# Kernel tuning notes

Hardware: AMD Instinct MI355X
Metric: run time of the kernel (lower is better)

## Reference

```python
import jax, jax.numpy as jnp
import numpy as np

B, C, N, M, K = 1, 64, 65536, 65536, 16
H, O = 64, 128  # mlp hidden, out_channels


def setup_inputs() -> dict:
    key = jax.random.key(0)
    ks = jax.random.split(key, 8)
    return {
        "x": jax.random.normal(ks[0], (B, C, N), dtype=jnp.float32),
        "pos": jax.random.normal(ks[1], (B, 3, N), dtype=jnp.float32),
        "support_points": jax.random.normal(ks[2], (B, 3, M), dtype=jnp.float32),
        "W1": jax.random.normal(ks[3], (H, C + 3), dtype=jnp.float32) * 0.05,
        "b1": jax.random.normal(ks[4], (H,), dtype=jnp.float32) * 0.05,
        "W2": jax.random.normal(ks[5], (O, H), dtype=jnp.float32) * 0.05,
        "b2": jax.random.normal(ks[6], (O,), dtype=jnp.float32) * 0.05,
        "indices": jax.random.randint(ks[7], (B, M, K), 0, N, dtype=jnp.int64),
    }


def _gather_points(t, indices):
    # t: [B, C, N], indices: [B, M, K] -> [B, C, M, K]
    b, c, n = t.shape
    m, k = indices.shape[1], indices.shape[2]
    idx = indices.reshape(b, 1, m * k)  # broadcasts over channel dim
    return jnp.take_along_axis(t, idx, axis=2).reshape(b, c, m, k)


def reference(x, pos, support_points, W1, b1, W2, b2, indices):
    # gather neighbor features and positions: [B, C, M, K], [B, 3, M, K]
    feats = _gather_points(x, indices)
    pts = _gather_points(pos, indices) - support_points[:, :, :, None]
    h = jnp.concatenate([feats, pts], axis=1)  # [B, C+3, M, K]
    # shared per-point MLP (1x1 Conv2d == channel contraction)
    h = jnp.einsum("oc,bcmk->bomk", W1, h) + b1[None, :, None, None]
    h = jax.nn.relu(h)
    h = jnp.einsum("oc,bcmk->bomk", W2, h) + b2[None, :, None, None]
    # max-pool over neighborhood K -> [B, O, M]
    return jnp.max(h, axis=3)
```

## Files before the change

kernel.cpp:

```cpp
#include <hip/hip_runtime.h>
#include <hip/hip_bf16.h>

#define NPTS 65536
#define MPTS 65536

typedef __attribute__((ext_vector_type(8))) short bf16x8;
typedef __attribute__((ext_vector_type(4))) float f32x4;

__device__ __forceinline__ float bflo(unsigned int u){ union{unsigned int i; float f;} v; v.i = u<<16; return v.f; }
__device__ __forceinline__ float bfhi(unsigned int u){ union{unsigned int i; float f;} v; v.i = u & 0xffff0000u; return v.f; }
__device__ __forceinline__ unsigned short f2bf(float f){
  union{float f; unsigned int i;} v; v.f=f;
  unsigned int r = v.i + 0x7fffu + ((v.i>>16)&1u);
  return (unsigned short)(r>>16);
}
__device__ __forceinline__ unsigned int pk2f(float a, float b){
  float2 tf; tf.x = a; tf.y = b;
  union { __hip_bfloat162 h; unsigned int u; } c;
  c.h = __float22bfloat162_rn(tf);
  return c.u;
}

#define MFMA32(a,b,c) __builtin_amdgcn_mfma_f32_16x16x32_bf16((a),(b),(c),0,0,0)

__global__ __launch_bounds__(256) void pack_u(
    const float* __restrict__ x,
    const float* __restrict__ pos,
    const float* __restrict__ sup,
    const float* __restrict__ W1,
    const float* __restrict__ b1,
    const float* __restrict__ W2,
    unsigned short* __restrict__ U,
    unsigned short* __restrict__ W2F,
    float* __restrict__ V) {
  const int t = threadIdx.x;
  if (blockIdx.x >= 1028) {
    const int m = (blockIdx.x - 1028) * 256 + t;
    const float s0 = sup[m], s1 = sup[MPTS + m], s2 = sup[2*MPTS + m];
    #pragma unroll
    for (int cg = 0; cg < 16; ++cg) {
      const float* r0 = W1 + (size_t)(cg*4 + 0)*67 + 64;
      const float* r1 = W1 + (size_t)(cg*4 + 1)*67 + 64;
      const float* r2 = W1 + (size_t)(cg*4 + 2)*67 + 64;
      const float* r3 = W1 + (size_t)(cg*4 + 3)*67 + 64;
      float4 o;
      o.x = r0[0]*s0 + r0[1]*s1 + r0[2]*s2;
      o.y = r1[0]*s0 + r1[1]*s1 + r1[2]*s2;
      o.z = r2[0]*s0 + r2[1]*s1 + r2[2]*s2;
      o.w = r3[0]*s0 + r3[1]*s1 + r3[2]*s2;
      *(float4*)(V + (size_t)m*64 + cg*4) = o;
    }
    return;
  }
  if (blockIdx.x >= 1024) {
    const int gg = (blockIdx.x - 1024) * 256 + t;
    if (gg < 1024) {
      const int g = gg >> 6, lane = gg & 63;
      const int q = lane >> 4, lr = lane & 15;
      const int kt = g >> 3, ot = g & 7;
      #pragma unroll
      for (int j = 0; j < 4; ++j)
        *(unsigned int*)&W2F[gg*8 + 2*j] =
            pk2f(W2[(ot*16 + lr)*64 + kt*32 + q*8 + 2*j],
                 W2[(ot*16 + lr)*64 + kt*32 + q*8 + 2*j + 1]);
    }
    return;
  }
  const int lane = t & 63, w = t >> 6, quad = lane >> 4, lr = lane & 15;
  const int n = blockIdx.x * 64 + w * 16 + lr;

  bf16x8 wa[2][4], wt[4];
  #pragma unroll
  for (int kt = 0; kt < 2; ++kt)
    #pragma unroll
    for (int nt = 0; nt < 4; ++nt) {
      const float* r = W1 + (size_t)(nt*16 + lr)*67 + kt*32 + quad*8;
      const float4 a = *(const float4*)r;
      const float4 b = *(const float4*)(r + 4);
      union { unsigned int d[4]; bf16x8 v; } mk;
      mk.d[0] = pk2f(a.x, a.y); mk.d[1] = pk2f(a.z, a.w);
      mk.d[2] = pk2f(b.x, b.y); mk.d[3] = pk2f(b.z, b.w);
      wa[kt][nt] = mk.v;
    }
  #pragma unroll
  for (int nt = 0; nt < 4; ++nt) {
    union { unsigned int d[4]; bf16x8 v; } mk;
    mk.d[0] = 0u; mk.d[1] = 0u; mk.d[2] = 0u; mk.d[3] = 0u;
    if (quad == 0) {
      const float* r = W1 + (size_t)(nt*16 + lr)*67 + 64;
      mk.d[0] = pk2f(r[0], r[1]);
      mk.d[1] = (unsigned int)f2bf(r[2]);
    }
    wt[nt] = mk.v;
  }

  const f32x4 fz = {0.f, 0.f, 0.f, 0.f};
  f32x4 acc[4] = {fz, fz, fz, fz};
  #pragma unroll
  for (int kt = 0; kt < 2; ++kt) {
    const float* xc = x + (size_t)(kt*32 + quad*8) * NPTS + n;
    union { unsigned int d[4]; bf16x8 v; } mk;
    #pragma unroll
    for (int i = 0; i < 4; ++i)
      mk.d[i] = pk2f(xc[(size_t)(2*i) * NPTS], xc[(size_t)(2*i + 1) * NPTS]);
    #pragma unroll
    for (int nt = 0; nt < 4; ++nt)
      acc[nt] = MFMA32(wa[kt][nt], mk.v, acc[nt]);
  }
  {
    union { unsigned int d[4]; bf16x8 v; } mk;
    mk.d[0] = pk2f(pos[n], pos[NPTS + n]);
    mk.d[1] = (unsigned int)f2bf(pos[2*NPTS + n]);
    mk.d[2] = 0u; mk.d[3] = 0u;
    #pragma unroll
    for (int nt = 0; nt < 4; ++nt)
      acc[nt] = MFMA32(wt[nt], mk.v, acc[nt]);
  }
  #pragma unroll
  for (int nt = 0; nt < 4; ++nt) {
    const float4 bb = *(const float4*)(b1 + nt*16 + quad*4);
    uint2 d;
    d.x = pk2f(acc[nt][0] + bb.x, acc[nt][1] + bb.y);
    d.y = pk2f(acc[nt][2] + bb.z, acc[nt][3] + bb.w);
    *(uint2*)(U + (size_t)n * 64 + nt*16 + quad*4) = d;
  }
}

__global__ __launch_bounds__(256, 3) void pointnet_reg2(
    const unsigned short* __restrict__ U,
    const float* __restrict__ V,
    const unsigned short* __restrict__ W2F,
    const float* __restrict__ b2,
    const int* __restrict__ indices,
    float* __restrict__ out) {
  const int t = threadIdx.x;
  const int lane = t & 63, w = t >> 6, quad = lane >> 4, lr = lane & 15;
  const int wbase = blockIdx.x * 32 + w * 8;

  int idx[8];
  #pragma unroll
  for (int pt = 0; pt < 8; ++pt) idx[pt] = indices[(wbase + pt)*16 + lr];

  uint4 ur[8][2];
  #pragma unroll
  for (int pt = 0; pt < 8; ++pt)
    #pragma unroll
    for (int kt = 0; kt < 2; ++kt)
      ur[pt][kt] = *(const uint4*)(U + (size_t)idx[pt]*64 + kt*32 + quad*8);

  bf16x8 ah[8][2];
  #pragma unroll
  for (int pt = 0; pt < 8; ++pt) {
    const float* vr = V + (size_t)(wbase + pt)*64 + quad*8;
    float vv[16];
    *(float4*)&vv[0]  = *(const float4*)(vr);
    *(float4*)&vv[4]  = *(const float4*)(vr + 4);
    *(float4*)&vv[8]  = *(const float4*)(vr + 32);
    *(float4*)&vv[12] = *(const float4*)(vr + 36);
    #pragma unroll
    for (int kt = 0; kt < 2; ++kt) {
      const unsigned int uu[4] = {ur[pt][kt].x, ur[pt][kt].y, ur[pt][kt].z, ur[pt][kt].w};
      union { unsigned int d[4]; bf16x8 v; } mk;
      #pragma unroll
      for (int i = 0; i < 4; ++i) {
        const float lo = bflo(uu[i]) - vv[kt*8 + 2*i];
        const float hi = bfhi(uu[i]) - vv[kt*8 + 2*i + 1];
        mk.d[i] = pk2f(fmaxf(lo, 0.f), fmaxf(hi, 0.f));
      }
      ah[pt][kt] = mk.v;
    }
  }

  const f32x4 fz = {0.f, 0.f, 0.f, 0.f};
  #pragma unroll
  for (int ot = 0; ot < 8; ++ot) {
    const bf16x8 wb0 = ((const bf16x8*)W2F)[(0*8 + ot)*64 + lane];
    const bf16x8 wb1 = ((const bf16x8*)W2F)[(1*8 + ot)*64 + lane];
    float vm[8];
    #pragma unroll
    for (int pt = 0; pt < 8; ++pt) {
      f32x4 a2 = MFMA32(ah[pt][0], wb0, fz);
      a2 = MFMA32(ah[pt][1], wb1, a2);
      float v = fmaxf(fmaxf(a2[0], a2[1]), fmaxf(a2[2], a2[3]));
      v = fmaxf(v, __int_as_float(__builtin_amdgcn_ds_swizzle(__float_as_int(v), 0x401F)));
      v = fmaxf(v, __shfl_xor(v, 32));
      vm[pt] = v;
    }
    const int o = ot*16 + lr;
    const float bb = b2[o];
    const float va = (quad & 1) ? ((quad & 2) ? vm[3] : vm[1])
                                : ((quad & 2) ? vm[2] : vm[0]);
    const float vb = (quad & 1) ? ((quad & 2) ? vm[7] : vm[5])
                                : ((quad & 2) ? vm[6] : vm[4]);
    out[(size_t)o * MPTS + wbase + quad] = va + bb;
    out[(size_t)o * MPTS + wbase + 4 + quad] = vb + bb;
  }
}

__global__ __launch_bounds__(256, 3) void pointnet_reg(
    const unsigned short* __restrict__ U,
    const float* __restrict__ sup,
    const float* __restrict__ W1,
    const unsigned short* __restrict__ W2F,
    const float* __restrict__ b2,
    const int* __restrict__ indices,
    float* __restrict__ out) {
  const int t = threadIdx.x;
  const int lane = t & 63, w = t >> 6, quad = lane >> 4, lr = lane & 15;
  const int wbase = blockIdx.x * 32 + w * 8;

  int idx[8];
  #pragma unroll
  for (int pt = 0; pt < 8; ++pt) idx[pt] = indices[(wbase + pt)*16 + lr];

  uint4 ur[8][2];
  #pragma unroll
  for (int pt = 0; pt < 8; ++pt)
    #pragma unroll
    for (int kt = 0; kt < 2; ++kt)
      ur[pt][kt] = *(const uint4*)(U + (size_t)idx[pt]*64 + kt*32 + quad*8);

  bf16x8 ah[8][2];
  #pragma unroll
  for (int kt = 0; kt < 2; ++kt) {
    float w1p[8][3];
    #pragma unroll
    for (int j = 0; j < 8; ++j) {
      const float* r = W1 + (size_t)(kt*32 + quad*8 + j)*67 + 64;
      w1p[j][0] = r[0]; w1p[j][1] = r[1]; w1p[j][2] = r[2];
    }
    #pragma unroll
    for (int pt = 0; pt < 8; ++pt) {
      const float s0 = sup[wbase + pt];
      const float s1 = sup[MPTS + wbase + pt];
      const float s2 = sup[2*MPTS + wbase + pt];
      const unsigned int uu[4] = {ur[pt][kt].x, ur[pt][kt].y, ur[pt][kt].z, ur[pt][kt].w};
      union { unsigned int d[4]; bf16x8 v; } mk;
      #pragma unroll
      for (int i = 0; i < 4; ++i) {
        const float vl = w1p[2*i][0]*s0 + w1p[2*i][1]*s1 + w1p[2*i][2]*s2;
        const float vh = w1p[2*i+1][0]*s0 + w1p[2*i+1][1]*s1 + w1p[2*i+1][2]*s2;
        const float hl = fmaxf(bflo(uu[i]) - vl, 0.f);
        const float hh = fmaxf(bfhi(uu[i]) - vh, 0.f);
        mk.d[i] = pk2f(hl, hh);
      }
      ah[pt][kt] = mk.v;
    }
  }

  const f32x4 fz = {0.f, 0.f, 0.f, 0.f};
  #pragma unroll
  for (int ot = 0; ot < 8; ++ot) {
    const bf16x8 wb0 = ((const bf16x8*)W2F)[(0*8 + ot)*64 + lane];
    const bf16x8 wb1 = ((const bf16x8*)W2F)[(1*8 + ot)*64 + lane];
    float vm[8];
    #pragma unroll
    for (int pt = 0; pt < 8; ++pt) {
      f32x4 a2 = MFMA32(ah[pt][0], wb0, fz);
      a2 = MFMA32(ah[pt][1], wb1, a2);
      float v = fmaxf(fmaxf(a2[0], a2[1]), fmaxf(a2[2], a2[3]));
      v = fmaxf(v, __shfl_xor(v, 16));
      v = fmaxf(v, __shfl_xor(v, 32));
      vm[pt] = v;
    }
    const int o = ot*16 + lr;
    const float bb = b2[o];
    const float va = (quad & 1) ? ((quad & 2) ? vm[3] : vm[1])
                                : ((quad & 2) ? vm[2] : vm[0]);
    const float vb = (quad & 1) ? ((quad & 2) ? vm[7] : vm[5])
                                : ((quad & 2) ? vm[6] : vm[4]);
    out[(size_t)o * MPTS + wbase + quad] = va + bb;
    out[(size_t)o * MPTS + wbase + 4 + quad] = vb + bb;
  }
}

__global__ __launch_bounds__(256) void pointnet_fallback(
    const float* __restrict__ x, const float* __restrict__ pos,
    const float* __restrict__ sup,
    const float* __restrict__ W1, const float* __restrict__ b1,
    const float* __restrict__ W2, const float* __restrict__ b2,
    const int* __restrict__ indices, float* __restrict__ out) {
  __shared__ float sfeat[16][68];
  __shared__ float shid[16][64];
  __shared__ float smax[4][128];
  __shared__ int sidx[16];
  const int t = threadIdx.x;
  const int m = blockIdx.x;
  if (t < 16) sidx[t] = indices[m*16 + t];
  const float sup0 = sup[m], sup1 = sup[MPTS + m], sup2 = sup[2*MPTS + m];
  __syncthreads();
  for (int u = t; u < 16*17; u += 256) {
    const int k = u / 17, c4 = (u - k*17) * 4;
    const int idx = sidx[k];
    float4 wv;
    if (c4 < 64) {
      wv.x = x[(size_t)(c4+0)*NPTS + idx]; wv.y = x[(size_t)(c4+1)*NPTS + idx];
      wv.z = x[(size_t)(c4+2)*NPTS + idx]; wv.w = x[(size_t)(c4+3)*NPTS + idx];
    } else {
      wv.x = pos[idx] - sup0; wv.y = pos[NPTS + idx] - sup1;
      wv.z = pos[2*NPTS + idx] - sup2; wv.w = 0.f;
    }
    *(float4*)&sfeat[k][c4] = wv;
  }
  const int h = t & 63, kg = t >> 6;
  float w1r[68];
  #pragma unroll
  for (int c = 0; c < 67; ++c) w1r[c] = W1[h*67 + c];
  w1r[67] = 0.f;
  const float bias1 = b1[h];
  __syncthreads();
  #pragma unroll
  for (int j = 0; j < 4; ++j) {
    const int k = kg*4 + j;
    float a = bias1;
    const float4* rr = (const float4*)sfeat[k];
    #pragma unroll
    for (int qq = 0; qq < 17; ++qq) {
      const float4 v = rr[qq];
      a += w1r[qq*4+0]*v.x + w1r[qq*4+1]*v.y + w1r[qq*4+2]*v.z + w1r[qq*4+3]*v.w;
    }
    shid[k][h] = fmaxf(a, 0.f);
  }
  const int ow = t & 63;
  float w2a[64], w2b[64];
  #pragma unroll
  for (int hh = 0; hh < 64; ++hh) { w2a[hh] = W2[ow*64 + hh]; w2b[hh] = W2[(ow+64)*64 + hh]; }
  __syncthreads();
  float mxa = -3.0e38f, mxb = -3.0e38f;
  #pragma unroll
  for (int j = 0; j < 4; ++j) {
    const int k = kg*4 + j;
    const float4* hr = (const float4*)shid[k];
    float pa = 0.f, pb = 0.f;
    #pragma unroll
    for (int qq = 0; qq < 16; ++qq) {
      const float4 v = hr[qq];
      pa += w2a[qq*4+0]*v.x + w2a[qq*4+1]*v.y + w2a[qq*4+2]*v.z + w2a[qq*4+3]*v.w;
      pb += w2b[qq*4+0]*v.x + w2b[qq*4+1]*v.y + w2b[qq*4+2]*v.z + w2b[qq*4+3]*v.w;
    }
    mxa = fmaxf(mxa, pa); mxb = fmaxf(mxb, pb);
  }
  smax[kg][ow] = mxa; smax[kg][64 + ow] = mxb;
  __syncthreads();
  if (t < 128) {
    out[(size_t)t * MPTS + m] =
        fmaxf(fmaxf(smax[0][t], smax[1][t]), fmaxf(smax[2][t], smax[3][t])) + b2[t];
  }
}

extern "C" void kernel_launch(void* const* d_in, const int* in_sizes, int n_in,
                              void* d_out, int out_size, void* d_ws, size_t ws_size,
                              hipStream_t stream) {
  const float* x   = (const float*)d_in[0];
  const float* pos = (const float*)d_in[1];
  const float* sup = (const float*)d_in[2];
  const float* W1  = (const float*)d_in[3];
  const float* b1  = (const float*)d_in[4];
  const float* W2  = (const float*)d_in[5];
  const float* b2  = (const float*)d_in[6];
  const int* indices = (const int*)d_in[7];
  float* out = (float*)d_out;

  const size_t U_BYTES   = (size_t)NPTS * 64 * 2;
  const size_t W2F_BYTES = 16 * 64 * 8 * 2;
  const size_t V_BYTES   = (size_t)MPTS * 64 * 4;
  if (ws_size >= U_BYTES + W2F_BYTES + V_BYTES) {
    unsigned short* U   = (unsigned short*)d_ws;
    unsigned short* W2F = (unsigned short*)((char*)d_ws + U_BYTES);
    float* V            = (float*)((char*)d_ws + U_BYTES + W2F_BYTES);
    pack_u<<<1028 + 256, 256, 0, stream>>>(x, pos, sup, W1, b1, W2, U, W2F, V);
    pointnet_reg2<<<MPTS/32, 256, 0, stream>>>(U, V, W2F, b2, indices, out);
  } else if (ws_size >= U_BYTES + W2F_BYTES) {
    unsigned short* U   = (unsigned short*)d_ws;
    unsigned short* W2F = (unsigned short*)((char*)d_ws + U_BYTES);
    pack_u<<<1028, 256, 0, stream>>>(x, pos, sup, W1, b1, W2, U, W2F, nullptr);
    pointnet_reg<<<MPTS/32, 256, 0, stream>>>(U, sup, W1, W2F, b2, indices, out);
  } else {
    pointnet_fallback<<<MPTS, 256, 0, stream>>>(x, pos, sup, W1, b1, W2, b2, indices, out);
  }
}
```

Measured before the change: 139.9 us.

## Split pack kernel, stage x/V tiles through LDS, vectorize output stores

```diff
diff --git a/kernel.cpp b/kernel.cpp
--- a/kernel.cpp
+++ b/kernel.cpp
@@ -26,34 +26,98 @@
 __global__ __launch_bounds__(256) void pack_u(
     const float* __restrict__ x,
     const float* __restrict__ pos,
+    const float* __restrict__ W1,
+    const float* __restrict__ b1,
+    unsigned short* __restrict__ U)
+{
+  __shared__ float sx[67][65];
+  const int t = threadIdx.x;
+  const int n0 = blockIdx.x * 64;
+
+  #pragma unroll
+  for (int i = 0; i < 4; ++i) {
+    const int lin = i*256 + t, r = lin >> 4, c4 = (lin & 15) * 4;
+    const float4 v = *(const float4*)&x[(size_t)r * NPTS + n0 + c4];
+    *(float4*)&sx[r][c4] = v;
+  }
+  if (t < 48) {
+    const int lin = 1024 + t, r = lin >> 4, c4 = (lin & 15) * 4;
+    const float4 v = *(const float4*)&pos[(size_t)(r - 64) * NPTS + n0 + c4];
+    *(float4*)&sx[r][c4] = v;
+  }
+
+  const int lane = t & 63, w = t >> 6, quad = lane >> 4, lr = lane & 15;
+  const int col = w * 16 + lr;
+  const int n = n0 + col;
+
+  bf16x8 wa[2][4], wt[4];
+  #pragma unroll
+  for (int kt = 0; kt < 2; ++kt)
+    #pragma unroll
+    for (int nt = 0; nt < 4; ++nt) {
+      const float* r = W1 + (size_t)(nt*16 + lr)*67 + kt*32 + quad*8;
+      const float4 a = *(const float4*)r;
+      const float4 b = *(const float4*)(r + 4);
+      union { unsigned int d[4]; bf16x8 v; } mk;
+      mk.d[0] = pk2f(a.x, a.y); mk.d[1] = pk2f(a.z, a.w);
+      mk.d[2] = pk2f(b.x, b.y); mk.d[3] = pk2f(b.z, b.w);
+      wa[kt][nt] = mk.v;
+    }
+  #pragma unroll
+  for (int nt = 0; nt < 4; ++nt) {
+    union { unsigned int d[4]; bf16x8 v; } mk;
+    mk.d[0] = 0u; mk.d[1] = 0u; mk.d[2] = 0u; mk.d[3] = 0u;
+    if (quad == 0) {
+      const float* r = W1 + (size_t)(nt*16 + lr)*67 + 64;
+      mk.d[0] = pk2f(r[0], r[1]);
+      mk.d[1] = (unsigned int)f2bf(r[2]);
+    }
+    wt[nt] = mk.v;
+  }
+
+  __syncthreads();
+
+  const f32x4 fz = {0.f, 0.f, 0.f, 0.f};
+  f32x4 acc[4] = {fz, fz, fz, fz};
+  #pragma unroll
+  for (int kt = 0; kt < 2; ++kt) {
+    const int c0 = kt*32 + quad*8;
+    union { unsigned int d[4]; bf16x8 v; } mk;
+    #pragma unroll
+    for (int i = 0; i < 4; ++i)
+      mk.d[i] = pk2f(sx[c0 + 2*i][col], sx[c0 + 2*i + 1][col]);
+    #pragma unroll
+    for (int nt = 0; nt < 4; ++nt)
+      acc[nt] = MFMA32(wa[kt][nt], mk.v, acc[nt]);
+  }
+  {
+    union { unsigned int d[4]; bf16x8 v; } mk;
+    mk.d[0] = pk2f(sx[64][col], sx[65][col]);
+    mk.d[1] = (unsigned int)f2bf(sx[66][col]);
+    mk.d[2] = 0u; mk.d[3] = 0u;
+    #pragma unroll
+    for (int nt = 0; nt < 4; ++nt)
+      acc[nt] = MFMA32(wt[nt], mk.v, acc[nt]);
+  }
+  #pragma unroll
+  for (int nt = 0; nt < 4; ++nt) {
+    const float4 bb = *(const float4*)(b1 + nt*16 + quad*4);
+    uint2 d;
+    d.x = pk2f(acc[nt][0] + bb.x, acc[nt][1] + bb.y);
+    d.y = pk2f(acc[nt][2] + bb.z, acc[nt][3] + bb.w);
+    *(uint2*)(U + (size_t)n * 64 + nt*16 + quad*4) = d;
+  }
+}
+
+__global__ __launch_bounds__(256) void pack_aux(
     const float* __restrict__ sup,
     const float* __restrict__ W1,
-    const float* __restrict__ b1,
     const float* __restrict__ W2,
-    unsigned short* __restrict__ U,
-    unsigned short* __restrict__ W2F,
-    float* __restrict__ V) {
+    float* __restrict__ V,
+    unsigned short* __restrict__ W2F) {
   const int t = threadIdx.x;
-  if (blockIdx.x >= 1028) {
-    const int m = (blockIdx.x - 1028) * 256 + t;
-    const float s0 = sup[m], s1 = sup[MPTS + m], s2 = sup[2*MPTS + m];
-    #pragma unroll
-    for (int cg = 0; cg < 16; ++cg) {
-      const float* r0 = W1 + (size_t)(cg*4 + 0)*67 + 64;
-      const float* r1 = W1 + (size_t)(cg*4 + 1)*67 + 64;
-      const float* r2 = W1 + (size_t)(cg*4 + 2)*67 + 64;
-      const float* r3 = W1 + (size_t)(cg*4 + 3)*67 + 64;
-      float4 o;
-      o.x = r0[0]*s0 + r0[1]*s1 + r0[2]*s2;
-      o.y = r1[0]*s0 + r1[1]*s1 + r1[2]*s2;
-      o.z = r2[0]*s0 + r2[1]*s1 + r2[2]*s2;
-      o.w = r3[0]*s0 + r3[1]*s1 + r3[2]*s2;
-      *(float4*)(V + (size_t)m*64 + cg*4) = o;
-    }
-    return;
-  }
-  if (blockIdx.x >= 1024) {
-    const int gg = (blockIdx.x - 1024) * 256 + t;
+  if (blockIdx.x >= 256) {
+    const int gg = (blockIdx.x - 256) * 256 + t;
     if (gg < 1024) {
       const int g = gg >> 6, lane = gg & 63;
       const int q = lane >> 4, lr = lane & 15;
@@ -66,80 +130,48 @@
     }
     return;
   }
-  const int lane = t & 63, w = t >> 6, quad = lane >> 4, lr = lane & 15;
-  const int n = blockIdx.x * 64 + w * 16 + lr;
-
-  bf16x8 wa[2][4], wt[4];
-  #pragma unroll
-  for (int kt = 0; kt < 2; ++kt)
-    #pragma unroll
-    for (int nt = 0; nt < 4; ++nt) {
-      const float* r = W1 + (size_t)(nt*16 + lr)*67 + kt*32 + quad*8;
-      const float4 a = *(const float4*)r;
-      const float4 b = *(const float4*)(r + 4);
-      union { unsigned int d[4]; bf16x8 v; } mk;
-      mk.d[0] = pk2f(a.x, a.y); mk.d[1] = pk2f(a.z, a.w);
-      mk.d[2] = pk2f(b.x, b.y); mk.d[3] = pk2f(b.z, b.w);
-      wa[kt][nt] = mk.v;
-    }
-  #pragma unroll
-  for (int nt = 0; nt < 4; ++nt) {
-    union { unsigned int d[4]; bf16x8 v; } mk;
-    mk.d[0] = 0u; mk.d[1] = 0u; mk.d[2] = 0u; mk.d[3] = 0u;
-    if (quad == 0) {
-      const float* r = W1 + (size_t)(nt*16 + lr)*67 + 64;
-      mk.d[0] = pk2f(r[0], r[1]);
-      mk.d[1] = (unsigned int)f2bf(r[2]);
-    }
-    wt[nt] = mk.v;
-  }
-
-  const f32x4 fz = {0.f, 0.f, 0.f, 0.f};
-  f32x4 acc[4] = {fz, fz, fz, fz};
-  #pragma unroll
-  for (int kt = 0; kt < 2; ++kt) {
-    const float* xc = x + (size_t)(kt*32 + quad*8) * NPTS + n;
-    union { unsigned int d[4]; bf16x8 v; } mk;
-    #pragma unroll
-    for (int i = 0; i < 4; ++i)
-      mk.d[i] = pk2f(xc[(size_t)(2*i) * NPTS], xc[(size_t)(2*i + 1) * NPTS]);
-    #pragma unroll
-    for (int nt = 0; nt < 4; ++nt)
-      acc[nt] = MFMA32(wa[kt][nt], mk.v, acc[nt]);
-  }
-  {
-    union { unsigned int d[4]; bf16x8 v; } mk;
-    mk.d[0] = pk2f(pos[n], pos[NPTS + n]);
-    mk.d[1] = (unsigned int)f2bf(pos[2*NPTS + n]);
-    mk.d[2] = 0u; mk.d[3] = 0u;
-    #pragma unroll
-    for (int nt = 0; nt < 4; ++nt)
-      acc[nt] = MFMA32(wt[nt], mk.v, acc[nt]);
-  }
-  #pragma unroll
-  for (int nt = 0; nt < 4; ++nt) {
-    const float4 bb = *(const float4*)(b1 + nt*16 + quad*4);
-    uint2 d;
-    d.x = pk2f(acc[nt][0] + bb.x, acc[nt][1] + bb.y);
-    d.y = pk2f(acc[nt][2] + bb.z, acc[nt][3] + bb.w);
-    *(uint2*)(U + (size_t)n * 64 + nt*16 + quad*4) = d;
-  }
-}
-
-__global__ __launch_bounds__(256, 3) void pointnet_reg2(
+  if (V == nullptr) return;
+  const int m = blockIdx.x * 256 + t;
+  const float s0 = sup[m], s1 = sup[MPTS + m], s2 = sup[2*MPTS + m];
+  #pragma unroll
+  for (int cg = 0; cg < 16; ++cg) {
+    const float* r0 = W1 + (size_t)(cg*4 + 0)*67 + 64;
+    const float* r1 = W1 + (size_t)(cg*4 + 1)*67 + 64;
+    const float* r2 = W1 + (size_t)(cg*4 + 2)*67 + 64;
+    const float* r3 = W1 + (size_t)(cg*4 + 3)*67 + 64;
+    float4 o;
+    o.x = r0[0]*s0 + r0[1]*s1 + r0[2]*s2;
+    o.y = r1[0]*s0 + r1[1]*s1 + r1[2]*s2;
+    o.z = r2[0]*s0 + r2[1]*s1 + r2[2]*s2;
+    o.w = r3[0]*s0 + r3[1]*s1 + r3[2]*s2;
+    *(float4*)(V + (size_t)m*64 + cg*4) = o;
+  }
+}
+
+__global__ __launch_bounds__(256, 3) void pointnet_reg3(
     const unsigned short* __restrict__ U,
     const float* __restrict__ V,
     const unsigned short* __restrict__ W2F,
     const float* __restrict__ b2,
     const int* __restrict__ indices,
     float* __restrict__ out) {
+  __shared__ float sv[32][64];
   const int t = threadIdx.x;
   const int lane = t & 63, w = t >> 6, quad = lane >> 4, lr = lane & 15;
-  const int wbase = blockIdx.x * 32 + w * 8;
+  const int mbase = blockIdx.x * 32;
+  const int wbase = mbase + w * 8;
+
+  #pragma unroll
+  for (int i = 0; i < 2; ++i) {
+    const int lin = i*256 + t, r = lin >> 4, c4 = (lin & 15) * 4;
+    *(float4*)&sv[r][c4] = *(const float4*)&V[(size_t)(mbase + r)*64 + c4];
+  }
 
   int idx[8];
   #pragma unroll
   for (int pt = 0; pt < 8; ++pt) idx[pt] = indices[(wbase + pt)*16 + lr];
+
+  __syncthreads();
 
   uint4 ur[8][2];
   #pragma unroll
@@ -151,12 +183,13 @@
   bf16x8 ah[8][2];
   #pragma unroll
   for (int pt = 0; pt < 8; ++pt) {
-    const float* vr = V + (size_t)(wbase + pt)*64 + quad*8;
-    float vv[16];
-    *(float4*)&vv[0]  = *(const float4*)(vr);
-    *(float4*)&vv[4]  = *(const float4*)(vr + 4);
-    *(float4*)&vv[8]  = *(const float4*)(vr + 32);
-    *(float4*)&vv[12] = *(const float4*)(vr + 36);
+    const float* vr = &sv[w*8 + pt][quad*8];
+    const f32x4 v0 = *(const f32x4*)(vr);
+    const f32x4 v1 = *(const f32x4*)(vr + 4);
+    const f32x4 v2 = *(const f32x4*)(vr + 32);
+    const f32x4 v3 = *(const f32x4*)(vr + 36);
+    const float vv[16] = {v0[0],v0[1],v0[2],v0[3], v1[0],v1[1],v1[2],v1[3],
+                          v2[0],v2[1],v2[2],v2[3], v3[0],v3[1],v3[2],v3[3]};
     #pragma unroll
     for (int kt = 0; kt < 2; ++kt) {
       const unsigned int uu[4] = {ur[pt][kt].x, ur[pt][kt].y, ur[pt][kt].z, ur[pt][kt].w};
@@ -172,6 +205,7 @@
   }
 
   const f32x4 fz = {0.f, 0.f, 0.f, 0.f};
+  __builtin_amdgcn_s_setprio(1);
   #pragma unroll
   for (int ot = 0; ot < 8; ++ot) {
     const bf16x8 wb0 = ((const bf16x8*)W2F)[(0*8 + ot)*64 + lane];
@@ -188,13 +222,14 @@
     }
     const int o = ot*16 + lr;
     const float bb = b2[o];
-    const float va = (quad & 1) ? ((quad & 2) ? vm[3] : vm[1])
-                                : ((quad & 2) ? vm[2] : vm[0]);
-    const float vb = (quad & 1) ? ((quad & 2) ? vm[7] : vm[5])
-                                : ((quad & 2) ? vm[6] : vm[4]);
-    out[(size_t)o * MPTS + wbase + quad] = va + bb;
-    out[(size_t)o * MPTS + wbase + 4 + quad] = vb + bb;
-  }
+    const float e0 = (quad & 1) ? ((quad & 2) ? vm[6] : vm[2])
+                                : ((quad & 2) ? vm[4] : vm[0]);
+    const float e1 = (quad & 1) ? ((quad & 2) ? vm[7] : vm[3])
+                                : ((quad & 2) ? vm[5] : vm[1]);
+    float2 st; st.x = e0 + bb; st.y = e1 + bb;
+    *(float2*)&out[(size_t)o * MPTS + wbase + 2*quad] = st;
+  }
+  __builtin_amdgcn_s_setprio(0);
 }
 
 __global__ __launch_bounds__(256, 3) void pointnet_reg(
@@ -368,12 +403,14 @@
     unsigned short* U   = (unsigned short*)d_ws;
     unsigned short* W2F = (unsigned short*)((char*)d_ws + U_BYTES);
     float* V            = (float*)((char*)d_ws + U_BYTES + W2F_BYTES);
-    pack_u<<<1028 + 256, 256, 0, stream>>>(x, pos, sup, W1, b1, W2, U, W2F, V);
-    pointnet_reg2<<<MPTS/32, 256, 0, stream>>>(U, V, W2F, b2, indices, out);
+    pack_aux<<<260, 256, 0, stream>>>(sup, W1, W2, V, W2F);
+    pack_u<<<NPTS/64, 256, 0, stream>>>(x, pos, W1, b1, U);
+    pointnet_reg3<<<MPTS/32, 256, 0, stream>>>(U, V, W2F, b2, indices, out);
   } else if (ws_size >= U_BYTES + W2F_BYTES) {
     unsigned short* U   = (unsigned short*)d_ws;
     unsigned short* W2F = (unsigned short*)((char*)d_ws + U_BYTES);
-    pack_u<<<1028, 256, 0, stream>>>(x, pos, sup, W1, b1, W2, U, W2F, nullptr);
+    pack_aux<<<260, 256, 0, stream>>>(sup, W1, W2, nullptr, W2F);
+    pack_u<<<NPTS/64, 256, 0, stream>>>(x, pos, W1, b1, U);
     pointnet_reg<<<MPTS/32, 256, 0, stream>>>(U, sup, W1, W2F, b2, indices, out);
   } else {
     pointnet_fallback<<<MPTS, 256, 0, stream>>>(x, pos, sup, W1, b1, W2, b2, indices, out);
```

After: 136.8 us. -2.2%, faster.

## Stage x/pos tiles in LDS and split gather kernel into two point groups

Applied to the files above, without the earlier changes.

```diff
diff --git a/kernel.cpp b/kernel.cpp
--- a/kernel.cpp
+++ b/kernel.cpp
@@ -20,10 +20,16 @@
   c.h = __float22bfloat162_rn(tf);
   return c.u;
 }
+__device__ __forceinline__ float swz16(float x){
+  return __int_as_float(__builtin_amdgcn_ds_swizzle(__float_as_int(x), 0x401F));
+}
+__device__ __forceinline__ float red4(f32x4 a){
+  return fmaxf(fmaxf(a[0], a[1]), fmaxf(a[2], a[3]));
+}
 
 #define MFMA32(a,b,c) __builtin_amdgcn_mfma_f32_16x16x32_bf16((a),(b),(c),0,0,0)
 
-__global__ __launch_bounds__(256) void pack_u(
+__global__ __launch_bounds__(256) void pack_all(
     const float* __restrict__ x,
     const float* __restrict__ pos,
     const float* __restrict__ sup,
@@ -66,8 +72,23 @@
     }
     return;
   }
+  __shared__ float sx[67][65];
+  const int n0 = blockIdx.x * 64;
+  #pragma unroll
+  for (int i = 0; i < 4; ++i) {
+    const int lin = i*256 + t, r = lin >> 4, c4 = (lin & 15) * 4;
+    const float4 v = *(const float4*)&x[(size_t)r * NPTS + n0 + c4];
+    *(float4*)&sx[r][c4] = v;
+  }
+  if (t < 48) {
+    const int lin = 1024 + t, r = lin >> 4, c4 = (lin & 15) * 4;
+    const float4 v = *(const float4*)&pos[(size_t)(r - 64) * NPTS + n0 + c4];
+    *(float4*)&sx[r][c4] = v;
+  }
+
   const int lane = t & 63, w = t >> 6, quad = lane >> 4, lr = lane & 15;
-  const int n = blockIdx.x * 64 + w * 16 + lr;
+  const int col = w * 16 + lr;
+  const int n = n0 + col;
 
   bf16x8 wa[2][4], wt[4];
   #pragma unroll
@@ -94,23 +115,25 @@
     wt[nt] = mk.v;
   }
 
+  __syncthreads();
+
   const f32x4 fz = {0.f, 0.f, 0.f, 0.f};
   f32x4 acc[4] = {fz, fz, fz, fz};
   #pragma unroll
   for (int kt = 0; kt < 2; ++kt) {
-    const float* xc = x + (size_t)(kt*32 + quad*8) * NPTS + n;
+    const int c0 = kt*32 + quad*8;
     union { unsigned int d[4]; bf16x8 v; } mk;
     #pragma unroll
     for (int i = 0; i < 4; ++i)
-      mk.d[i] = pk2f(xc[(size_t)(2*i) * NPTS], xc[(size_t)(2*i + 1) * NPTS]);
+      mk.d[i] = pk2f(sx[c0 + 2*i][col], sx[c0 + 2*i + 1][col]);
     #pragma unroll
     for (int nt = 0; nt < 4; ++nt)
       acc[nt] = MFMA32(wa[kt][nt], mk.v, acc[nt]);
   }
   {
     union { unsigned int d[4]; bf16x8 v; } mk;
-    mk.d[0] = pk2f(pos[n], pos[NPTS + n]);
-    mk.d[1] = (unsigned int)f2bf(pos[2*NPTS + n]);
+    mk.d[0] = pk2f(sx[64][col], sx[65][col]);
+    mk.d[1] = (unsigned int)f2bf(sx[66][col]);
     mk.d[2] = 0u; mk.d[3] = 0u;
     #pragma unroll
     for (int nt = 0; nt < 4; ++nt)
@@ -126,75 +149,110 @@
   }
 }
 
-__global__ __launch_bounds__(256, 3) void pointnet_reg2(
+__global__ __launch_bounds__(256, 3) void pointnet_reg5(
     const unsigned short* __restrict__ U,
     const float* __restrict__ V,
     const unsigned short* __restrict__ W2F,
     const float* __restrict__ b2,
     const int* __restrict__ indices,
     float* __restrict__ out) {
+  __shared__ float sv[32][68];
   const int t = threadIdx.x;
   const int lane = t & 63, w = t >> 6, quad = lane >> 4, lr = lane & 15;
-  const int wbase = blockIdx.x * 32 + w * 8;
-
-  int idx[8];
-  #pragma unroll
-  for (int pt = 0; pt < 8; ++pt) idx[pt] = indices[(wbase + pt)*16 + lr];
-
-  uint4 ur[8][2];
-  #pragma unroll
-  for (int pt = 0; pt < 8; ++pt)
-    #pragma unroll
-    for (int kt = 0; kt < 2; ++kt)
-      ur[pt][kt] = *(const uint4*)(U + (size_t)idx[pt]*64 + kt*32 + quad*8);
-
-  bf16x8 ah[8][2];
-  #pragma unroll
-  for (int pt = 0; pt < 8; ++pt) {
-    const float* vr = V + (size_t)(wbase + pt)*64 + quad*8;
-    float vv[16];
-    *(float4*)&vv[0]  = *(const float4*)(vr);
-    *(float4*)&vv[4]  = *(const float4*)(vr + 4);
-    *(float4*)&vv[8]  = *(const float4*)(vr + 32);
-    *(float4*)&vv[12] = *(const float4*)(vr + 36);
-    #pragma unroll
-    for (int kt = 0; kt < 2; ++kt) {
-      const unsigned int uu[4] = {ur[pt][kt].x, ur[pt][kt].y, ur[pt][kt].z, ur[pt][kt].w};
-      union { unsigned int d[4]; bf16x8 v; } mk;
-      #pragma unroll
-      for (int i = 0; i < 4; ++i) {
-        const float lo = bflo(uu[i]) - vv[kt*8 + 2*i];
-        const float hi = bfhi(uu[i]) - vv[kt*8 + 2*i + 1];
-        mk.d[i] = pk2f(fmaxf(lo, 0.f), fmaxf(hi, 0.f));
-      }
-      ah[pt][kt] = mk.v;
-    }
-  }
+  const int mbase = blockIdx.x * 32;
+  const int wbase = mbase + w * 8;
+
+  int idx[2][4];
+  #pragma unroll
+  for (int g = 0; g < 2; ++g)
+    #pragma unroll
+    for (int p = 0; p < 4; ++p)
+      idx[g][p] = indices[(wbase + g*4 + p)*16 + lr];
+
+  const int vrow = w*8 + (lane >> 3), vcol = (lane & 7) * 8;
+  const float* vg = &V[(size_t)(mbase + vrow) * 64 + vcol];
+  const float4 vt0 = *(const float4*)(vg);
+  const float4 vt1 = *(const float4*)(vg + 4);
+
+  uint4 ur0[4][2], ur1[4][2];
+  #pragma unroll
+  for (int p = 0; p < 4; ++p) {
+    const size_t rowb = (size_t)idx[0][p] * 64;
+    ur0[p][0] = *(const uint4*)(U + rowb + quad*8);
+    ur0[p][1] = *(const uint4*)(U + rowb + 32 + quad*8);
+  }
+  #pragma unroll
+  for (int p = 0; p < 4; ++p) {
+    const size_t rowb = (size_t)idx[1][p] * 64;
+    ur1[p][0] = *(const uint4*)(U + rowb + quad*8);
+    ur1[p][1] = *(const uint4*)(U + rowb + 32 + quad*8);
+  }
+
+  *(float4*)&sv[vrow][vcol]     = vt0;
+  *(float4*)&sv[vrow][vcol + 4] = vt1;
+
+  float bias[8];
+  #pragma unroll
+  for (int ot = 0; ot < 8; ++ot) bias[ot] = b2[ot*16 + lr];
 
   const f32x4 fz = {0.f, 0.f, 0.f, 0.f};
-  #pragma unroll
-  for (int ot = 0; ot < 8; ++ot) {
-    const bf16x8 wb0 = ((const bf16x8*)W2F)[(0*8 + ot)*64 + lane];
-    const bf16x8 wb1 = ((const bf16x8*)W2F)[(1*8 + ot)*64 + lane];
-    float vm[8];
-    #pragma unroll
-    for (int pt = 0; pt < 8; ++pt) {
-      f32x4 a2 = MFMA32(ah[pt][0], wb0, fz);
-      a2 = MFMA32(ah[pt][1], wb1, a2);
-      float v = fmaxf(fmaxf(a2[0], a2[1]), fmaxf(a2[2], a2[3]));
-      v = fmaxf(v, __int_as_float(__builtin_amdgcn_ds_swizzle(__float_as_int(v), 0x401F)));
-      v = fmaxf(v, __shfl_xor(v, 32));
-      vm[pt] = v;
-    }
-    const int o = ot*16 + lr;
-    const float bb = b2[o];
-    const float va = (quad & 1) ? ((quad & 2) ? vm[3] : vm[1])
-                                : ((quad & 2) ? vm[2] : vm[0]);
-    const float vb = (quad & 1) ? ((quad & 2) ? vm[7] : vm[5])
-                                : ((quad & 2) ? vm[6] : vm[4]);
-    out[(size_t)o * MPTS + wbase + quad] = va + bb;
-    out[(size_t)o * MPTS + wbase + 4 + quad] = vb + bb;
-  }
+  const bf16x8* W2Fv = (const bf16x8*)W2F;
+
+#define PN_GROUP(g, CUR)                                                        \
+  {                                                                             \
+    bf16x8 ah[4][2];                                                            \
+    _Pragma("unroll")                                                           \
+    for (int p = 0; p < 4; ++p) {                                               \
+      const float* vr = &sv[w*8 + (g)*4 + p][quad*8];                           \
+      const f32x4 v0 = *(const f32x4*)(vr);                                     \
+      const f32x4 v1 = *(const f32x4*)(vr + 4);                                 \
+      const f32x4 v2 = *(const f32x4*)(vr + 32);                                \
+      const f32x4 v3 = *(const f32x4*)(vr + 36);                                \
+      const float vv[16] = {v0[0],v0[1],v0[2],v0[3], v1[0],v1[1],v1[2],v1[3],   \
+                            v2[0],v2[1],v2[2],v2[3], v3[0],v3[1],v3[2],v3[3]};  \
+      _Pragma("unroll")                                                         \
+      for (int kt = 0; kt < 2; ++kt) {                                          \
+        const unsigned int uu[4] = {CUR[p][kt].x, CUR[p][kt].y,                 \
+                                    CUR[p][kt].z, CUR[p][kt].w};                \
+        union { unsigned int d[4]; bf16x8 v; } mk;                              \
+        _Pragma("unroll")                                                       \
+        for (int i = 0; i < 4; ++i) {                                           \
+          const float lo = bflo(uu[i]) - vv[kt*8 + 2*i];                        \
+          const float hi = bfhi(uu[i]) - vv[kt*8 + 2*i + 1];                    \
+          mk.d[i] = pk2f(fmaxf(lo, 0.f), fmaxf(hi, 0.f));                       \
+        }                                                                       \
+        ah[p][kt] = mk.v;                                                       \
+      }                                                                         \
+    }                                                                           \
+    _Pragma("unroll")                                                           \
+    for (int ot = 0; ot < 8; ++ot) {                                            \
+      const bf16x8 wb0 = W2Fv[(0*8 + ot)*64 + lane];                            \
+      const bf16x8 wb1 = W2Fv[(1*8 + ot)*64 + lane];                            \
+      f32x4 aA, aB;                                                             \
+      aA = MFMA32(ah[0][0], wb0, fz); aA = MFMA32(ah[0][1], wb1, aA);           \
+      aB = MFMA32(ah[1][0], wb0, fz); aB = MFMA32(ah[1][1], wb1, aB);           \
+      float q0 = red4(aA);                                                      \
+      aA = MFMA32(ah[2][0], wb0, fz); aA = MFMA32(ah[2][1], wb1, aA);           \
+      float q1 = red4(aB);                                                      \
+      aB = MFMA32(ah[3][0], wb0, fz); aB = MFMA32(ah[3][1], wb1, aB);           \
+      float q2 = red4(aA);                                                      \
+      float q3 = red4(aB);                                                      \
+      float u0 = swz16(q0), u1 = swz16(q1), u2 = swz16(q2), u3 = swz16(q3);     \
+      q0 = fmaxf(q0, u0); q1 = fmaxf(q1, u1);                                   \
+      q2 = fmaxf(q2, u2); q3 = fmaxf(q3, u3);                                   \
+      u0 = __shfl_xor(q0, 32); u1 = __shfl_xor(q1, 32);                         \
+      u2 = __shfl_xor(q2, 32); u3 = __shfl_xor(q3, 32);                         \
+      q0 = fmaxf(q0, u0); q1 = fmaxf(q1, u1);                                   \
+      q2 = fmaxf(q2, u2); q3 = fmaxf(q3, u3);                                   \
+      const float e = (quad & 1) ? ((quad & 2) ? q3 : q1)                       \
+                                 : ((quad & 2) ? q2 : q0);                      \
+      out[(size_t)(ot*16 + lr) * MPTS + wbase + (g)*4 + quad] = e + bias[ot];   \
+    }                                                                           \
+  }
+
+  PN_GROUP(0, ur0)
+  PN_GROUP(1, ur1)
+#undef PN_GROUP
 }
 
 __global__ __launch_bounds__(256, 3) void pointnet_reg(
@@ -368,12 +426,12 @@
     unsigned short* U   = (unsigned short*)d_ws;
     unsigned short* W2F = (unsigned short*)((char*)d_ws + U_BYTES);
     float* V            = (float*)((char*)d_ws + U_BYTES + W2F_BYTES);
-    pack_u<<<1028 + 256, 256, 0, stream>>>(x, pos, sup, W1, b1, W2, U, W2F, V);
-    pointnet_reg2<<<MPTS/32, 256, 0, stream>>>(U, V, W2F, b2, indices, out);
+    pack_all<<<1284, 256, 0, stream>>>(x, pos, sup, W1, b1, W2, U, W2F, V);
+    pointnet_reg5<<<MPTS/32, 256, 0, stream>>>(U, V, W2F, b2, indices, out);
   } else if (ws_size >= U_BYTES + W2F_BYTES) {
     unsigned short* U   = (unsigned short*)d_ws;
     unsigned short* W2F = (unsigned short*)((char*)d_ws + U_BYTES);
-    pack_u<<<1028, 256, 0, stream>>>(x, pos, sup, W1, b1, W2, U, W2F, nullptr);
+    pack_all<<<1028, 256, 0, stream>>>(x, pos, sup, W1, b1, W2, U, W2F, nullptr);
     pointnet_reg<<<MPTS/32, 256, 0, stream>>>(U, sup, W1, W2F, b2, indices, out);
   } else {
     pointnet_fallback<<<MPTS, 256, 0, stream>>>(x, pos, sup, W1, b1, W2, b2, indices, out);
```

After: 142.3 us. Within noise of the previous version (+1.7%).
